# Optimization experiments

Hardware: AMD Instinct MI355X
Metric: run time of the kernel (lower is better)

Reference implementation:

```python
import jax, jax.numpy as jnp
import numpy as np

NUM_HEADS = 14
NUM_KV_HEADS = 2
HEAD_DIM = 64
HIDDEN = 896
ROPE_THETA = 1000000.0
NEG_INF = -1e9


def _rope_tables(seq_len, dtype=jnp.float32):
    inv_freq = 1.0 / (ROPE_THETA ** (jnp.arange(0, HEAD_DIM, 2, dtype=jnp.float32) / HEAD_DIM))
    t = jnp.arange(seq_len, dtype=jnp.float32)
    freqs = t[:, None] * inv_freq[None, :]          # [S, hd/2]
    emb = jnp.concatenate((freqs, freqs), axis=-1)  # [S, hd]
    return jnp.cos(emb).astype(dtype), jnp.sin(emb).astype(dtype)


def _rotate_half(x):
    x1, x2 = x[..., : x.shape[-1] // 2], x[..., x.shape[-1] // 2 :]
    return jnp.concatenate((-x2, x1), axis=-1)


def setup_inputs() -> dict:
    key = jax.random.key(0)
    ks = jax.random.split(key, 6)
    B, S = 2, 2048
    hidden_states = jax.random.normal(ks[0], (B, S, HIDDEN), dtype=jnp.float32)
    # additive causal mask [1, 1, S, S]
    causal = jnp.tril(jnp.ones((S, S), dtype=bool))
    attention_mask = jnp.where(causal, 0.0, NEG_INF).astype(jnp.float32)[None, None]
    sd = 1.0 / np.sqrt(HIDDEN)
    Wq = jax.random.normal(ks[1], (HIDDEN, NUM_HEADS * HEAD_DIM), dtype=jnp.float32) * sd
    bq = jnp.zeros((NUM_HEADS * HEAD_DIM,), dtype=jnp.float32)
    Wk = jax.random.normal(ks[2], (HIDDEN, NUM_KV_HEADS * HEAD_DIM), dtype=jnp.float32) * sd
    bk = jnp.zeros((NUM_KV_HEADS * HEAD_DIM,), dtype=jnp.float32)
    Wv = jax.random.normal(ks[3], (HIDDEN, NUM_KV_HEADS * HEAD_DIM), dtype=jnp.float32) * sd
    bv = jnp.zeros((NUM_KV_HEADS * HEAD_DIM,), dtype=jnp.float32)
    Wo = jax.random.normal(ks[4], (NUM_HEADS * HEAD_DIM, HIDDEN), dtype=jnp.float32) * sd
    return {
        'hidden_states': hidden_states, 'attention_mask': attention_mask,
        'Wq': Wq, 'bq': bq, 'Wk': Wk, 'bk': bk, 'Wv': Wv, 'bv': bv, 'Wo': Wo,
    }


def reference(hidden_states, attention_mask, Wq, bq, Wk, bk, Wv, bv, Wo):
    B, S, _ = hidden_states.shape
    n_groups = NUM_HEADS // NUM_KV_HEADS
    q = (hidden_states @ Wq + bq).reshape(B, S, NUM_HEADS, HEAD_DIM)
    k = (hidden_states @ Wk + bk).reshape(B, S, NUM_KV_HEADS, HEAD_DIM)
    v = (hidden_states @ Wv + bv).reshape(B, S, NUM_KV_HEADS, HEAD_DIM)

    cos, sin = _rope_tables(S, hidden_states.dtype)
    cos = cos[None, :, None, :]
    sin = sin[None, :, None, :]
    q = q * cos + _rotate_half(q) * sin
    k = k * cos + _rotate_half(k) * sin

    # GQA: repeat kv heads to match query heads
    k = jnp.repeat(k, n_groups, axis=2)  # [B, S, nH, hd]
    v = jnp.repeat(v, n_groups, axis=2)

    q = q.transpose(0, 2, 1, 3)  # [B, nH, S, hd]
    k = k.transpose(0, 2, 1, 3)
    v = v.transpose(0, 2, 1, 3)

    scores = jnp.einsum('bhqd,bhkd->bhqk', q, k) / jnp.sqrt(jnp.float32(HEAD_DIM)).astype(q.dtype)
    scores = scores + attention_mask
    attn = jax.nn.softmax(scores, axis=-1)
    out = jnp.einsum('bhqk,bhkd->bhqd', attn, v)        # [B, nH, S, hd]
    out = out.transpose(0, 2, 1, 3).reshape(B, S, -1)   # [B, S, nH*hd]
    return out @ Wo
```

## Files before the change

### kernel.cpp

```cpp
#include <hip/hip_runtime.h>
#include <hip/hip_bf16.h>
#include <math.h>

#define NH 14
#define NKV 2
#define HD 64
#define HID 896
#define SEQ 2048
#define BATCH 2
#define KT 28

typedef __attribute__((ext_vector_type(8))) short short8;
typedef __attribute__((ext_vector_type(4))) float f32x4;
typedef unsigned short ushort_t;

__device__ __forceinline__ unsigned short f2b(float f) {
    unsigned int u = __float_as_uint(f);
    unsigned int r = (u + 0x7fffu + ((u >> 16) & 1u)) >> 16;
    return (unsigned short)r;
}

__device__ __forceinline__ float exp2fast(float x) {
    return __builtin_amdgcn_exp2f(x);
}

__device__ __forceinline__ void gload16(const ushort_t* g, ushort_t* l) {
    __builtin_amdgcn_global_load_lds(
        (const __attribute__((address_space(1))) void*)g,
        (__attribute__((address_space(3))) void*)l,
        16, 0, 0);
}

__global__ __launch_bounds__(256) void xcast_kernel(
    const float* __restrict__ X, ushort_t* __restrict__ Xb)
{
    size_t i = ((size_t)blockIdx.x * 256 + threadIdx.x) * 8;
    float4 a = *(const float4*)(X + i);
    float4 b = *(const float4*)(X + i + 4);
    short8 o;
    o[0] = f2b(a.x); o[1] = f2b(a.y); o[2] = f2b(a.z); o[3] = f2b(a.w);
    o[4] = f2b(b.x); o[5] = f2b(b.y); o[6] = f2b(b.z); o[7] = f2b(b.w);
    *(short8*)(Xb + i) = o;
}

__global__ __launch_bounds__(256) void wtrans_kernel(
    const float* __restrict__ Wq, const float* __restrict__ Wk,
    const float* __restrict__ Wv, const float* __restrict__ Wo,
    ushort_t* __restrict__ WqkvT, ushort_t* __restrict__ WoT)
{
    __shared__ float tile[32][33];
    const int tx = threadIdx.x, ty = threadIdx.y;
    const int z = blockIdx.z;
    const float* src; ushort_t* dst; int N, rowoff;
    if      (z == 0) { src = Wq; dst = WqkvT; N = HID; rowoff = 0;    }
    else if (z == 1) { src = Wk; dst = WqkvT; N = 128; rowoff = 896;  }
    else if (z == 2) { src = Wv; dst = WqkvT; N = 128; rowoff = 1024; }
    else             { src = Wo; dst = WoT;   N = HID; rowoff = 0;    }
    const int k0 = blockIdx.x * 32;
    const int n0 = blockIdx.y * 32;
    if (n0 >= N) return;
    #pragma unroll
    for (int i = 0; i < 4; ++i)
        tile[ty * 4 + i][tx] = src[(size_t)(k0 + ty * 4 + i) * N + n0 + tx];
    __syncthreads();
    #pragma unroll
    for (int i = 0; i < 4; ++i)
        dst[(size_t)(rowoff + n0 + ty * 4 + i) * HID + k0 + tx]
            = f2b(tile[tx][ty * 4 + i]);
}

__global__ __launch_bounds__(256) void qkv_kernel(
    const ushort_t* __restrict__ Xb, const ushort_t* __restrict__ WqkvT,
    const float* __restrict__ bq, const float* __restrict__ bk,
    const float* __restrict__ bv,
    ushort_t* __restrict__ qbuf, ushort_t* __restrict__ kbuf,
    ushort_t* __restrict__ vbuf)
{
    __shared__ ushort_t Asb[2][128 * 32];
    __shared__ ushort_t Bsb[2][64 * 32];
    const int tid  = threadIdx.x;
    const int w    = tid >> 6;
    const int lane = tid & 63;
    const int quad = lane >> 4;
    const int l16  = lane & 15;
    const int m0 = blockIdx.x * 128;
    const int nt = blockIdx.y;
    const int nb = nt * 64;

    const int srow = lane >> 2;
    const int scol = (lane & 3) * 8;
    const ushort_t* gA0 = Xb + (size_t)(m0 + w * 32 + srow) * HID + scol;
    const ushort_t* gA1 = gA0 + (size_t)16 * HID;
    const ushort_t* gB  = WqkvT + (size_t)(nb + w * 16 + srow) * HID + scol;

    #define QKV_ISSUE(buf, ks)                                        \
        do {                                                          \
            gload16(gA0 + (ks) * 32, &Asb[buf][(w * 32) * 32]);       \
            gload16(gA1 + (ks) * 32, &Asb[buf][(w * 32 + 16) * 32]);  \
            gload16(gB  + (ks) * 32, &Bsb[buf][(w * 16) * 32]);       \
        } while (0)

    f32x4 acc[2][4];
    #pragma unroll
    for (int mf = 0; mf < 2; ++mf)
        #pragma unroll
        for (int nf = 0; nf < 4; ++nf) acc[mf][nf] = (f32x4){0.f, 0.f, 0.f, 0.f};

    QKV_ISSUE(0, 0);
    QKV_ISSUE(1, 1);

    for (int ks = 0; ks < KT; ++ks) {
        const int cur = ks & 1;
        if (ks + 1 < KT) asm volatile("s_waitcnt vmcnt(3)" ::: "memory");
        else             asm volatile("s_waitcnt vmcnt(0)" ::: "memory");
        __builtin_amdgcn_s_barrier();
        asm volatile("" ::: "memory");
        const ushort_t* Ab = &Asb[cur][(w * 32 + l16) * 32 + quad * 8];
        short8 a0 = *(const short8*)Ab;
        short8 a1 = *(const short8*)(Ab + 16 * 32);
        #pragma unroll
        for (int nf = 0; nf < 4; ++nf) {
            short8 bf = *(const short8*)&Bsb[cur][(nf * 16 + l16) * 32 + quad * 8];
            acc[0][nf] = __builtin_amdgcn_mfma_f32_16x16x32_bf16(a0, bf, acc[0][nf], 0, 0, 0);
            acc[1][nf] = __builtin_amdgcn_mfma_f32_16x16x32_bf16(a1, bf, acc[1][nf], 0, 0, 0);
        }
        asm volatile("" ::: "memory");
        __builtin_amdgcn_s_barrier();
        if (ks + 2 < KT) QKV_ISSUE(cur, ks + 2);
    }
    #undef QKV_ISSUE

    float bcol[4];
    #pragma unroll
    for (int f = 0; f < 4; ++f) {
        int d = f * 16 + l16;
        bcol[f] = (nt < 14) ? bq[nt * 64 + d]
                : (nt < 16) ? bk[(nt - 14) * 64 + d]
                            : bv[(nt - 16) * 64 + d];
    }
    const float lnth = 13.815510558f;
    float if0 = expf(-((float)l16)        / 32.0f * lnth);
    float if1 = expf(-((float)(l16 + 16)) / 32.0f * lnth);

    #pragma unroll
    for (int mf = 0; mf < 2; ++mf)
        #pragma unroll
        for (int r = 0; r < 4; ++r) {
            int grow = m0 + w * 32 + mf * 16 + quad * 4 + r;
            int b = grow >> 11;
            int s = grow & 2047;
            float v0 = acc[mf][0][r] + bcol[0];
            float v1 = acc[mf][1][r] + bcol[1];
            float v2 = acc[mf][2][r] + bcol[2];
            float v3 = acc[mf][3][r] + bcol[3];
            if (nt < 16) {
                float s0, c0, s1, c1;
                sincosf((float)s * if0, &s0, &c0);
                sincosf((float)s * if1, &s1, &c1);
                float n0 = v0 * c0 - v2 * s0;
                float n2 = v2 * c0 + v0 * s0;
                float n1 = v1 * c1 - v3 * s1;
                float n3 = v3 * c1 + v1 * s1;
                v0 = n0; v1 = n1; v2 = n2; v3 = n3;
            }
            if (nt < 14) {
                const float qs = 0.18033688f;
                v0 *= qs; v1 *= qs; v2 *= qs; v3 *= qs;
                ushort_t* dst = qbuf + ((size_t)(b * NH + nt) * SEQ + s) * HD;
                dst[l16]      = f2b(v0);
                dst[l16 + 16] = f2b(v1);
                dst[l16 + 32] = f2b(v2);
                dst[l16 + 48] = f2b(v3);
            } else if (nt < 16) {
                ushort_t* dst = kbuf + ((size_t)(b * NKV + nt - 14) * SEQ + s) * HD;
                dst[l16]      = f2b(v0);
                dst[l16 + 16] = f2b(v1);
                dst[l16 + 32] = f2b(v2);
                dst[l16 + 48] = f2b(v3);
            } else {
                ushort_t* dst = vbuf + (size_t)(b * NKV + nt - 16) * HD * SEQ + s;
                dst[(size_t)(l16)      * SEQ] = f2b(v0);
                dst[(size_t)(l16 + 16) * SEQ] = f2b(v1);
                dst[(size_t)(l16 + 32) * SEQ] = f2b(v2);
                dst[(size_t)(l16 + 48) * SEQ] = f2b(v3);
            }
        }
}

#define LDP 76
#define SMMAX 12.0f
__global__ __launch_bounds__(256, 4) void attn_kernel(
    const ushort_t* __restrict__ qbuf, const ushort_t* __restrict__ kbuf,
    const ushort_t* __restrict__ vbuf, ushort_t* __restrict__ abuf)
{
    __shared__ ushort_t Ks[64 * LDP];
    __shared__ ushort_t Vt[64 * LDP];
    __shared__ ushort_t Ps[4][32 * LDP];

    const int tid  = threadIdx.x;
    const int w    = tid >> 6;
    const int lane = tid & 63;
    const int quad = lane >> 4;
    const int l16  = lane & 15;
    const int qt = ((blockIdx.y + blockIdx.z) & 1) ? blockIdx.x
                                                   : (15 - blockIdx.x);
    const int h  = blockIdx.y;
    const int b  = blockIdx.z;
    const int kvh = h / (NH / NKV);

    const ushort_t* kb_h = kbuf + (size_t)(b * NKV + kvh) * SEQ * HD;
    const ushort_t* vt_h = vbuf + (size_t)(b * NKV + kvh) * HD * SEQ;

    const int srow = tid >> 3;
    const int sc8  = tid & 7;
    const ushort_t* Kg0 = kb_h + (size_t)srow * HD + sc8 * 8;
    const ushort_t* Kg1 = kb_h + (size_t)(srow + 32) * HD + sc8 * 8;
    const ushort_t* Vg0 = vt_h + (size_t)srow * SEQ + sc8 * 8;
    const ushort_t* Vg1 = vt_h + (size_t)(srow + 32) * SEQ + sc8 * 8;

    const ushort_t* qbase =
        qbuf + ((size_t)((b * NH + h) * SEQ) + qt * 128 + w * 16 + l16) * HD;
    short8 qa0 = *(const short8*)(qbase + quad * 8);
    short8 qa1 = *(const short8*)(qbase + 32 + quad * 8);
    short8 qb0 = *(const short8*)(qbase + (size_t)64 * HD + quad * 8);
    short8 qb1 = *(const short8*)(qbase + (size_t)64 * HD + 32 + quad * 8);

    short8 onesb;
    #pragma unroll
    for (int i = 0; i < 8; ++i) onesb[i] = (short)0x3F80;

    f32x4 O0[4], O1[4], La0, La1;
    #pragma unroll
    for (int n = 0; n < 4; ++n) {
        O0[n] = (f32x4){0.f, 0.f, 0.f, 0.f};
        O1[n] = (f32x4){0.f, 0.f, 0.f, 0.f};
    }
    La0 = (f32x4){0.f, 0.f, 0.f, 0.f};
    La1 = (f32x4){0.f, 0.f, 0.f, 0.f};

    const int ktmax = 2 * qt + 1;

    short8 kr0 = *(const short8*)(Kg0);
    short8 kr1 = *(const short8*)(Kg1);
    short8 vr0 = *(const short8*)(Vg0);
    short8 vr1 = *(const short8*)(Vg1);

    for (int kt = 0; kt <= ktmax; ++kt) {
        __syncthreads();
        *(short8*)&Ks[srow * LDP + sc8 * 8]        = kr0;
        *(short8*)&Ks[(srow + 32) * LDP + sc8 * 8] = kr1;
        *(short8*)&Vt[srow * LDP + sc8 * 8]        = vr0;
        *(short8*)&Vt[(srow + 32) * LDP + sc8 * 8] = vr1;
        __syncthreads();
        if (kt < ktmax) {
            kr0 = *(const short8*)(Kg0 + (size_t)(kt + 1) * 64 * HD);
            kr1 = *(const short8*)(Kg1 + (size_t)(kt + 1) * 64 * HD);
            vr0 = *(const short8*)(Vg0 + (kt + 1) * 64);
            vr1 = *(const short8*)(Vg1 + (kt + 1) * 64);
        }

        const bool act0  = (kt <= 2 * qt);
        const bool diag0 = (kt == 2 * qt);
        const bool diag1 = (kt == ktmax);

        #pragma unroll
        for (int f = 0; f < 4; ++f) {
            short8 kf0 = *(const short8*)&Ks[(f * 16 + l16) * LDP + quad * 8];
            short8 kf1 = *(const short8*)&Ks[(f * 16 + l16) * LDP + 32 + quad * 8];
            f32x4 s1 = (f32x4){0.f, 0.f, 0.f, 0.f};
            s1 = __builtin_amdgcn_mfma_f32_16x16x32_bf16(qb0, kf0, s1, 0, 0, 0);
            s1 = __builtin_amdgcn_mfma_f32_16x16x32_bf16(qb1, kf1, s1, 0, 0, 0);
            f32x4 s0 = (f32x4){0.f, 0.f, 0.f, 0.f};
            if (act0) {
                s0 = __builtin_amdgcn_mfma_f32_16x16x32_bf16(qa0, kf0, s0, 0, 0, 0);
                s0 = __builtin_amdgcn_mfma_f32_16x16x32_bf16(qa1, kf1, s0, 0, 0, 0);
            }
            #pragma unroll
            for (int r = 0; r < 4; ++r) {
                float v1 = s1[r];
                if (diag1 && (f * 16 + l16) > (w * 16 + quad * 4 + r)) v1 = -1e30f;
                Ps[w][(16 + quad * 4 + r) * LDP + f * 16 + l16]
                    = f2b(exp2fast(v1 - SMMAX));
            }
            if (act0) {
                #pragma unroll
                for (int r = 0; r < 4; ++r) {
                    float v0 = s0[r];
                    if (diag0 && (f * 16 + l16) > (w * 16 + quad * 4 + r)) v0 = -1e30f;
                    Ps[w][(quad * 4 + r) * LDP + f * 16 + l16]
                        = f2b(exp2fast(v0 - SMMAX));
                }
            }
        }

        short8 pa1_0 = *(const short8*)&Ps[w][(16 + l16) * LDP + quad * 8];
        short8 pa1_1 = *(const short8*)&Ps[w][(16 + l16) * LDP + 32 + quad * 8];
        La1 = __builtin_amdgcn_mfma_f32_16x16x32_bf16(pa1_0, onesb, La1, 0, 0, 0);
        La1 = __builtin_amdgcn_mfma_f32_16x16x32_bf16(pa1_1, onesb, La1, 0, 0, 0);
        short8 pa0_0 = pa1_0, pa0_1 = pa1_1;
        if (act0) {
            pa0_0 = *(const short8*)&Ps[w][l16 * LDP + quad * 8];
            pa0_1 = *(const short8*)&Ps[w][l16 * LDP + 32 + quad * 8];
            La0 = __builtin_amdgcn_mfma_f32_16x16x32_bf16(pa0_0, onesb, La0, 0, 0, 0);
            La0 = __builtin_amdgcn_mfma_f32_16x16x32_bf16(pa0_1, onesb, La0, 0, 0, 0);
        }

        #pragma unroll
        for (int n = 0; n < 4; ++n) {
            short8 vf0 = *(const short8*)&Vt[(n * 16 + l16) * LDP + quad * 8];
            short8 vf1 = *(const short8*)&Vt[(n * 16 + l16) * LDP + 32 + quad * 8];
            O1[n] = __builtin_amdgcn_mfma_f32_16x16x32_bf16(pa1_0, vf0, O1[n], 0, 0, 0);
            O1[n] = __builtin_amdgcn_mfma_f32_16x16x32_bf16(pa1_1, vf1, O1[n], 0, 0, 0);
            if (act0) {
                O0[n] = __builtin_amdgcn_mfma_f32_16x16x32_bf16(pa0_0, vf0, O0[n], 0, 0, 0);
                O0[n] = __builtin_amdgcn_mfma_f32_16x16x32_bf16(pa0_1, vf1, O0[n], 0, 0, 0);
            }
        }
    }

    float inv0[4], inv1[4];
    #pragma unroll
    for (int r = 0; r < 4; ++r) { inv0[r] = 1.0f / La0[r]; inv1[r] = 1.0f / La1[r]; }
    #pragma unroll
    for (int n = 0; n < 4; ++n)
        #pragma unroll
        for (int r = 0; r < 4; ++r) {
            int rowg0 = qt * 128 + w * 16 + quad * 4 + r;
            abuf[(size_t)(b * SEQ + rowg0) * HID + h * HD + n * 16 + l16]
                = f2b(O0[n][r] * inv0[r]);
            abuf[(size_t)(b * SEQ + rowg0 + 64) * HID + h * HD + n * 16 + l16]
                = f2b(O1[n][r] * inv1[r]);
        }
}

__global__ __launch_bounds__(256) void oproj_kernel(
    const ushort_t* __restrict__ A, const ushort_t* __restrict__ WoT,
    float* __restrict__ out)
{
    __shared__ ushort_t Asb[2][128 * 32];
    __shared__ ushort_t Bsb[2][64 * 32];
    const int tid  = threadIdx.x;
    const int w    = tid >> 6;
    const int lane = tid & 63;
    const int quad = lane >> 4;
    const int l16  = lane & 15;
    const int m0 = blockIdx.x * 128;
    const int n0 = blockIdx.y * 64;

    const int srow = lane >> 2;
    const int scol = (lane & 3) * 8;
    const ushort_t* gA0 = A + (size_t)(m0 + w * 32 + srow) * HID + scol;
    const ushort_t* gA1 = gA0 + (size_t)16 * HID;
    const ushort_t* gB  = WoT + (size_t)(n0 + w * 16 + srow) * HID + scol;

    #define OP_ISSUE(buf, ks)                                         \
        do {                                                          \
            gload16(gA0 + (ks) * 32, &Asb[buf][(w * 32) * 32]);       \
            gload16(gA1 + (ks) * 32, &Asb[buf][(w * 32 + 16) * 32]);  \
            gload16(gB  + (ks) * 32, &Bsb[buf][(w * 16) * 32]);       \
        } while (0)

    f32x4 acc[2][4];
    #pragma unroll
    for (int mf = 0; mf < 2; ++mf)
        #pragma unroll
        for (int nf = 0; nf < 4; ++nf) acc[mf][nf] = (f32x4){0.f, 0.f, 0.f, 0.f};

    OP_ISSUE(0, 0);
    OP_ISSUE(1, 1);

    for (int ks = 0; ks < KT; ++ks) {
        const int cur = ks & 1;
        if (ks + 1 < KT) asm volatile("s_waitcnt vmcnt(3)" ::: "memory");
        else             asm volatile("s_waitcnt vmcnt(0)" ::: "memory");
        __builtin_amdgcn_s_barrier();
        asm volatile("" ::: "memory");
        const ushort_t* Ab = &Asb[cur][(w * 32 + l16) * 32 + quad * 8];
        short8 a0 = *(const short8*)Ab;
        short8 a1 = *(const short8*)(Ab + 16 * 32);
        #pragma unroll
        for (int nf = 0; nf < 4; ++nf) {
            short8 bf = *(const short8*)&Bsb[cur][(nf * 16 + l16) * 32 + quad * 8];
            acc[0][nf] = __builtin_amdgcn_mfma_f32_16x16x32_bf16(a0, bf, acc[0][nf], 0, 0, 0);
            acc[1][nf] = __builtin_amdgcn_mfma_f32_16x16x32_bf16(a1, bf, acc[1][nf], 0, 0, 0);
        }
        asm volatile("" ::: "memory");
        __builtin_amdgcn_s_barrier();
        if (ks + 2 < KT) OP_ISSUE(cur, ks + 2);
    }
    #undef OP_ISSUE

    #pragma unroll
    for (int mf = 0; mf < 2; ++mf)
        #pragma unroll
        for (int r = 0; r < 4; ++r) {
            size_t rbase = (size_t)(m0 + w * 32 + mf * 16 + quad * 4 + r) * HID + n0;
            #pragma unroll
            for (int f = 0; f < 4; ++f)
                out[rbase + f * 16 + l16] = acc[mf][f][r];
        }
}

extern "C" void kernel_launch(void* const* d_in, const int* in_sizes, int n_in,
                              void* d_out, int out_size, void* d_ws, size_t ws_size,
                              hipStream_t stream) {
    const float* X  = (const float*)d_in[0];
    const float* Wq = (const float*)d_in[2];
    const float* bq = (const float*)d_in[3];
    const float* Wk = (const float*)d_in[4];
    const float* bk = (const float*)d_in[5];
    const float* Wv = (const float*)d_in[6];
    const float* bv = (const float*)d_in[7];
    const float* Wo = (const float*)d_in[8];
    float* out = (float*)d_out;

    ushort_t* ws    = (ushort_t*)d_ws;
    ushort_t* Xb    = ws;
    ushort_t* WqkvT = Xb    + 3670016;
    ushort_t* WoT   = WqkvT + 1032192;
    ushort_t* qbuf  = WoT   + 802816;
    ushort_t* kbuf  = qbuf  + 3670016;
    ushort_t* vbuf  = kbuf  + 524288;
    ushort_t* abufb = vbuf  + 524288;

    xcast_kernel<<<dim3(1792), 256, 0, stream>>>(X, Xb);
    wtrans_kernel<<<dim3(28, 28, 4), dim3(32, 8), 0, stream>>>(
        Wq, Wk, Wv, Wo, WqkvT, WoT);
    qkv_kernel<<<dim3(32, 18), 256, 0, stream>>>(
        Xb, WqkvT, bq, bk, bv, qbuf, kbuf, vbuf);
    attn_kernel<<<dim3(16, NH, BATCH), 256, 0, stream>>>(
        qbuf, kbuf, vbuf, abufb);
    oproj_kernel<<<dim3(32, 14), 256, 0, stream>>>(
        abufb, WoT, out);
}
```

Baseline: 178.5 us.

## Split causal attention KV range across two blocks and combine partials

Adds a split-KV attention kernel in which each query tile's key range is divided between two blocks, which doubles the grid and balances the causal work. Each block writes unnormalized fp32 partial outputs and row sums, and a separate combine kernel adds the two halves, normalizes, and writes bf16 into the projection input. The path is used only when the workspace is large enough. It costs extra fp32 global traffic and one more kernel launch.

```diff
diff --git a/kernel.cpp b/kernel.cpp
--- a/kernel.cpp
+++ b/kernel.cpp
@@ -11,6 +11,7 @@
 #define KT 28
 
 typedef __attribute__((ext_vector_type(8))) short short8;
+typedef __attribute__((ext_vector_type(4))) short short4v;
 typedef __attribute__((ext_vector_type(4))) float f32x4;
 typedef unsigned short ushort_t;
 
@@ -189,6 +190,176 @@
 
 #define LDP 76
 #define SMMAX 12.0f
+
+__global__ __launch_bounds__(256, 4) void attn_split_kernel(
+    const ushort_t* __restrict__ qbuf, const ushort_t* __restrict__ kbuf,
+    const ushort_t* __restrict__ vbuf,
+    float* __restrict__ Opart, float* __restrict__ Lpart)
+{
+    __shared__ ushort_t Ks[64 * LDP];
+    __shared__ ushort_t Vt[64 * LDP];
+    __shared__ ushort_t Ps[4][32 * LDP];
+
+    const int tid  = threadIdx.x;
+    const int w    = tid >> 6;
+    const int lane = tid & 63;
+    const int quad = lane >> 4;
+    const int l16  = lane & 15;
+    const int qt = 15 - (blockIdx.x >> 1);
+    const int sp = blockIdx.x & 1;
+    const int h  = blockIdx.y;
+    const int b  = blockIdx.z;
+    const int kvh = h / (NH / NKV);
+
+    const int ktlo = sp ? (qt + 1) : 0;
+    const int kthi = sp ? (2 * qt + 1) : qt;
+
+    const ushort_t* kb_h = kbuf + (size_t)(b * NKV + kvh) * SEQ * HD;
+    const ushort_t* vt_h = vbuf + (size_t)(b * NKV + kvh) * HD * SEQ;
+
+    const int srow = tid >> 3;
+    const int sc8  = tid & 7;
+    const ushort_t* Kg0 = kb_h + (size_t)srow * HD + sc8 * 8;
+    const ushort_t* Kg1 = kb_h + (size_t)(srow + 32) * HD + sc8 * 8;
+    const ushort_t* Vg0 = vt_h + (size_t)srow * SEQ + sc8 * 8;
+    const ushort_t* Vg1 = vt_h + (size_t)(srow + 32) * SEQ + sc8 * 8;
+
+    const ushort_t* qbase =
+        qbuf + ((size_t)((b * NH + h) * SEQ) + qt * 128 + w * 16 + l16) * HD;
+    short8 qa0 = *(const short8*)(qbase + quad * 8);
+    short8 qa1 = *(const short8*)(qbase + 32 + quad * 8);
+    short8 qb0 = *(const short8*)(qbase + (size_t)64 * HD + quad * 8);
+    short8 qb1 = *(const short8*)(qbase + (size_t)64 * HD + 32 + quad * 8);
+
+    short8 onesb;
+    #pragma unroll
+    for (int i = 0; i < 8; ++i) onesb[i] = (short)0x3F80;
+
+    f32x4 O0[4], O1[4], La0, La1;
+    #pragma unroll
+    for (int n = 0; n < 4; ++n) {
+        O0[n] = (f32x4){0.f, 0.f, 0.f, 0.f};
+        O1[n] = (f32x4){0.f, 0.f, 0.f, 0.f};
+    }
+    La0 = (f32x4){0.f, 0.f, 0.f, 0.f};
+    La1 = (f32x4){0.f, 0.f, 0.f, 0.f};
+
+    short8 kr0 = *(const short8*)(Kg0 + (size_t)ktlo * 64 * HD);
+    short8 kr1 = *(const short8*)(Kg1 + (size_t)ktlo * 64 * HD);
+    short8 vr0 = *(const short8*)(Vg0 + ktlo * 64);
+    short8 vr1 = *(const short8*)(Vg1 + ktlo * 64);
+
+    for (int kt = ktlo; kt <= kthi; ++kt) {
+        __syncthreads();
+        *(short8*)&Ks[srow * LDP + sc8 * 8]        = kr0;
+        *(short8*)&Ks[(srow + 32) * LDP + sc8 * 8] = kr1;
+        *(short8*)&Vt[srow * LDP + sc8 * 8]        = vr0;
+        *(short8*)&Vt[(srow + 32) * LDP + sc8 * 8] = vr1;
+        __syncthreads();
+        if (kt < kthi) {
+            kr0 = *(const short8*)(Kg0 + (size_t)(kt + 1) * 64 * HD);
+            kr1 = *(const short8*)(Kg1 + (size_t)(kt + 1) * 64 * HD);
+            vr0 = *(const short8*)(Vg0 + (kt + 1) * 64);
+            vr1 = *(const short8*)(Vg1 + (kt + 1) * 64);
+        }
+
+        const bool act0  = (kt <= 2 * qt);
+        const bool diag0 = (kt == 2 * qt);
+        const bool diag1 = (kt == 2 * qt + 1);
+
+        #pragma unroll
+        for (int f = 0; f < 4; ++f) {
+            short8 kf0 = *(const short8*)&Ks[(f * 16 + l16) * LDP + quad * 8];
+            short8 kf1 = *(const short8*)&Ks[(f * 16 + l16) * LDP + 32 + quad * 8];
+            f32x4 s1 = (f32x4){0.f, 0.f, 0.f, 0.f};
+            s1 = __builtin_amdgcn_mfma_f32_16x16x32_bf16(qb0, kf0, s1, 0, 0, 0);
+            s1 = __builtin_amdgcn_mfma_f32_16x16x32_bf16(qb1, kf1, s1, 0, 0, 0);
+            f32x4 s0 = (f32x4){0.f, 0.f, 0.f, 0.f};
+            if (act0) {
+                s0 = __builtin_amdgcn_mfma_f32_16x16x32_bf16(qa0, kf0, s0, 0, 0, 0);
+                s0 = __builtin_amdgcn_mfma_f32_16x16x32_bf16(qa1, kf1, s0, 0, 0, 0);
+            }
+            #pragma unroll
+            for (int r = 0; r < 4; ++r) {
+                float v1 = s1[r];
+                if (diag1 && (f * 16 + l16) > (w * 16 + quad * 4 + r)) v1 = -1e30f;
+                Ps[w][(16 + quad * 4 + r) * LDP + f * 16 + l16]
+                    = f2b(exp2fast(v1 - SMMAX));
+            }
+            if (act0) {
+                #pragma unroll
+                for (int r = 0; r < 4; ++r) {
+                    float v0 = s0[r];
+                    if (diag0 && (f * 16 + l16) > (w * 16 + quad * 4 + r)) v0 = -1e30f;
+                    Ps[w][(quad * 4 + r) * LDP + f * 16 + l16]
+                        = f2b(exp2fast(v0 - SMMAX));
+                }
+            }
+        }
+
+        short8 pa1_0 = *(const short8*)&Ps[w][(16 + l16) * LDP + quad * 8];
+        short8 pa1_1 = *(const short8*)&Ps[w][(16 + l16) * LDP + 32 + quad * 8];
+        La1 = __builtin_amdgcn_mfma_f32_16x16x32_bf16(pa1_0, onesb, La1, 0, 0, 0);
+        La1 = __builtin_amdgcn_mfma_f32_16x16x32_bf16(pa1_1, onesb, La1, 0, 0, 0);
+        short8 pa0_0 = pa1_0, pa0_1 = pa1_1;
+        if (act0) {
+            pa0_0 = *(const short8*)&Ps[w][l16 * LDP + quad * 8];
+            pa0_1 = *(const short8*)&Ps[w][l16 * LDP + 32 + quad * 8];
+            La0 = __builtin_amdgcn_mfma_f32_16x16x32_bf16(pa0_0, onesb, La0, 0, 0, 0);
+            La0 = __builtin_amdgcn_mfma_f32_16x16x32_bf16(pa0_1, onesb, La0, 0, 0, 0);
+        }
+
+        #pragma unroll
+        for (int n = 0; n < 4; ++n) {
+            short8 vf0 = *(const short8*)&Vt[(n * 16 + l16) * LDP + quad * 8];
+            short8 vf1 = *(const short8*)&Vt[(n * 16 + l16) * LDP + 32 + quad * 8];
+            O1[n] = __builtin_amdgcn_mfma_f32_16x16x32_bf16(pa1_0, vf0, O1[n], 0, 0, 0);
+            O1[n] = __builtin_amdgcn_mfma_f32_16x16x32_bf16(pa1_1, vf1, O1[n], 0, 0, 0);
+            if (act0) {
+                O0[n] = __builtin_amdgcn_mfma_f32_16x16x32_bf16(pa0_0, vf0, O0[n], 0, 0, 0);
+                O0[n] = __builtin_amdgcn_mfma_f32_16x16x32_bf16(pa0_1, vf1, O0[n], 0, 0, 0);
+            }
+        }
+    }
+
+    float* Op = Opart + ((((size_t)sp * BATCH + b) * NH + h) * SEQ) * HD;
+    float* Lp = Lpart + (((size_t)sp * BATCH + b) * NH + h) * SEQ;
+    #pragma unroll
+    for (int n = 0; n < 4; ++n)
+        #pragma unroll
+        for (int r = 0; r < 4; ++r) {
+            int rowg0 = qt * 128 + w * 16 + quad * 4 + r;
+            Op[(size_t)rowg0 * HD + n * 16 + l16]        = O0[n][r];
+            Op[(size_t)(rowg0 + 64) * HD + n * 16 + l16] = O1[n][r];
+            if (n == 0 && l16 == 0) {
+                Lp[rowg0]      = La0[r];
+                Lp[rowg0 + 64] = La1[r];
+            }
+        }
+}
+
+__global__ __launch_bounds__(256) void combine_kernel(
+    const float* __restrict__ Opart, const float* __restrict__ Lpart,
+    ushort_t* __restrict__ abuf)
+{
+    const size_t HALF = (size_t)BATCH * NH * SEQ * HD;
+    size_t i = ((size_t)blockIdx.x * 256 + threadIdx.x) * 4;
+    f32x4 o0 = *(const f32x4*)(Opart + i);
+    f32x4 o1 = *(const f32x4*)(Opart + HALF + i);
+    size_t li = i >> 6;
+    float l = Lpart[li] + Lpart[(HALF >> 6) + li];
+    float inv = 1.0f / l;
+    int d0  = (int)(i & 63);
+    size_t rest = i >> 6;
+    int row = (int)(rest & 2047);
+    int bh  = (int)(rest >> 11);
+    int h = bh % NH, b = bh / NH;
+    short4v st;
+    #pragma unroll
+    for (int j = 0; j < 4; ++j) st[j] = (short)f2b((o0[j] + o1[j]) * inv);
+    *(short4v*)&abuf[((size_t)(b * SEQ + row)) * HID + h * HD + d0] = st;
+}
+
 __global__ __launch_bounds__(256, 4) void attn_kernel(
     const ushort_t* __restrict__ qbuf, const ushort_t* __restrict__ kbuf,
     const ushort_t* __restrict__ vbuf, ushort_t* __restrict__ abuf)
@@ -422,14 +593,26 @@
     ushort_t* kbuf  = qbuf  + 3670016;
     ushort_t* vbuf  = kbuf  + 524288;
     ushort_t* abufb = vbuf  + 524288;
+    float*    Opart = (float*)(abufb + 3670016);
+    float*    Lpart = Opart + 2 * 3670016;
+    const size_t WS_NEEDED =
+        (size_t)(3670016 + 1032192 + 802816 + 3670016 + 524288 + 524288
+                 + 3670016) * 2
+        + (size_t)(2 * 3670016 + 2 * 57344) * 4;
 
     xcast_kernel<<<dim3(1792), 256, 0, stream>>>(X, Xb);
     wtrans_kernel<<<dim3(28, 28, 4), dim3(32, 8), 0, stream>>>(
         Wq, Wk, Wv, Wo, WqkvT, WoT);
     qkv_kernel<<<dim3(32, 18), 256, 0, stream>>>(
         Xb, WqkvT, bq, bk, bv, qbuf, kbuf, vbuf);
-    attn_kernel<<<dim3(16, NH, BATCH), 256, 0, stream>>>(
-        qbuf, kbuf, vbuf, abufb);
+    if (ws_size >= WS_NEEDED) {
+        attn_split_kernel<<<dim3(32, NH, BATCH), 256, 0, stream>>>(
+            qbuf, kbuf, vbuf, Opart, Lpart);
+        combine_kernel<<<dim3(3584), 256, 0, stream>>>(Opart, Lpart, abufb);
+    } else {
+        attn_kernel<<<dim3(16, NH, BATCH), 256, 0, stream>>>(
+            qbuf, kbuf, vbuf, abufb);
+    }
     oproj_kernel<<<dim3(32, 14), 256, 0, stream>>>(
         abufb, WoT, out);
 }
```

After: 189.2 us. +6.0%, slower.
